# Performance work log

Hardware: AMD Instinct MI355X
Metric: run time of the kernel (lower is better)

Reference implementation:

```python
import jax, jax.numpy as jnp
import numpy as np

E = 128       # embedding_size
H = 4         # num_heads
D = E // H    # head_dim = 32
PAD = 16      # window_size; full window width = 2*PAD+1 = 33
B = 4
N = 8192


def setup_inputs() -> dict:
    key = jax.random.key(0)
    ks = jax.random.split(key, 9)
    s = 1.0 / np.sqrt(E)
    return {
        "q": jax.random.normal(ks[0], (B, N, E), dtype=jnp.float32),
        "Wq_w": jax.random.normal(ks[1], (E, E), dtype=jnp.float32) * s,
        "Wq_b": jax.random.normal(ks[2], (E,), dtype=jnp.float32) * s,
        "Wk_w": jax.random.normal(ks[3], (E, E), dtype=jnp.float32) * s,
        "Wk_b": jax.random.normal(ks[4], (E,), dtype=jnp.float32) * s,
        "Wv_w": jax.random.normal(ks[5], (E, E), dtype=jnp.float32) * s,
        "Wv_b": jax.random.normal(ks[6], (E,), dtype=jnp.float32) * s,
        "Wo_w": jax.random.normal(ks[7], (E, E), dtype=jnp.float32) * s,
        "Wo_b": jax.random.normal(ks[8], (E,), dtype=jnp.float32) * s,
    }


def reference(q, Wq_w, Wq_b, Wk_w, Wk_b, Wv_w, Wv_b, Wo_w, Wo_b):
    # Self-attention: k = v = q (forward defaults).
    Q = q @ Wq_w.T + Wq_b
    K = q @ Wk_w.T + Wk_b
    V = q @ Wv_w.T + Wv_b
    b, n, _ = Q.shape
    # (b, H, n, D)
    Q = Q.reshape(b, n, H, D).transpose(0, 2, 1, 3)
    K = K.reshape(b, n, H, D).transpose(0, 2, 1, 3)
    V = V.reshape(b, n, H, D).transpose(0, 2, 1, 3)
    W = 2 * PAD + 1
    # Zero-pad the sequence dim (matches F.pad: padded keys are zero vectors,
    # included in softmax WITHOUT masking — faithful to the original).
    K_pad = jnp.pad(K, ((0, 0), (0, 0), (PAD, PAD), (0, 0)))
    V_pad = jnp.pad(V, ((0, 0), (0, 0), (PAD, PAD), (0, 0)))
    # Window gather indices: row n sees padded positions n .. n+2*PAD
    idx = jnp.arange(n)[:, None] + jnp.arange(W)[None, :]  # (n, W)
    K_win = K_pad[:, :, idx]  # (b, H, n, W, D)
    V_win = V_pad[:, :, idx]  # (b, H, n, W, D)
    scores = jnp.einsum("bhnd,bhnwd->bhnw", Q, K_win) / jnp.sqrt(
        jnp.asarray(D, dtype=Q.dtype)
    )
    probs = jax.nn.softmax(scores, axis=-1)  # dropout is identity in eval
    out = jnp.einsum("bhnw,bhnwd->bhnd", probs, V_win)
    out = out.transpose(0, 2, 1, 3).reshape(b, n, E)
    out = out @ Wo_w.T + Wo_b
    return out, probs
```

## Files before the change

kernel.cpp:

```cpp
#include <hip/hip_runtime.h>

#define BN 4
#define NN 8192
#define EE 128
#define HH 4
#define DD 32
#define WW 33
#define MROWS (BN*NN)
#define QELEMS (MROWS*EE)
#define WELEMS (EE*EE)

typedef __bf16 bf16x8 __attribute__((ext_vector_type(8)));
typedef float f32x4 __attribute__((ext_vector_type(4)));
typedef unsigned short u16x8 __attribute__((ext_vector_type(8)));

static __device__ __forceinline__ unsigned short f2bf(float x){
    unsigned u = __float_as_uint(x);
    u += 0x7fffu + ((u >> 16) & 1u);
    return (unsigned short)(u >> 16);
}
static __device__ __forceinline__ float bf2f(unsigned short h){
    return __uint_as_float(((unsigned)h) << 16);
}
static __device__ __forceinline__ bf16x8 ld_bf8(const unsigned short* p){
    u16x8 v = *(const u16x8*)p;
    return __builtin_bit_cast(bf16x8, v);
}

__global__ void __launch_bounds__(256) prep_w(const float* __restrict__ wq, const float* __restrict__ wk,
        const float* __restrict__ wv, const float* __restrict__ wo,
        unsigned short* __restrict__ wh, unsigned short* __restrict__ wl){
    int i = blockIdx.x*256 + threadIdx.x;
    int sel = i >> 14;
    const float* src = (sel==0)? wq : (sel==1)? wk : (sel==2)? wv : wo;
    float x = src[i & (WELEMS-1)];
    unsigned short h = f2bf(x);
    wh[i] = h;
    wl[i] = f2bf(x - bf2f(h));
}

__global__ void __launch_bounds__(512,2) fused_kernel(
        const float* __restrict__ q,
        const unsigned short* __restrict__ wh, const unsigned short* __restrict__ wl,
        const float* __restrict__ bq, const float* __restrict__ bk, const float* __restrict__ bv_,
        const float* __restrict__ bo,
        float* __restrict__ out, float* __restrict__ probs)
{
    __shared__ float Kl[HH*96*33];
    __shared__ float Vl[HH*96*33];
    __shared__ float Ql[HH*64*33];

    const int t = threadIdx.x;
    const int wv = t >> 6;
    const int lane = t & 63;
    const int m = lane & 15, g = lane >> 4;
    const int b = blockIdx.y;
    const int n0 = blockIdx.x * 64;
    const size_t qrow0 = (size_t)b * NN;

    bf16x8 bH[3][4], bL[3][4];
    #pragma unroll
    for (int i=0;i<3;i++){
        const unsigned short* WH = wh + i*WELEMS + (size_t)(wv*16+m)*EE;
        const unsigned short* WL = wl + i*WELEMS + (size_t)(wv*16+m)*EE;
        #pragma unroll
        for (int kc=0;kc<4;kc++){
            bH[i][kc] = ld_bf8(WH + kc*32 + g*8);
            bL[i][kc] = ld_bf8(WL + kc*32 + g*8);
        }
    }
    const float bias3[3] = { bq[wv*16+m], bk[wv*16+m], bv_[wv*16+m] };
    const int head = wv >> 1, dimb = (wv & 1) * 16;

    float4 fa[2][8];
    {
        int grow = n0 - 16 + m;
        bool ok = (grow >= 0) && (grow < NN);
        const float* qp = q + (qrow0 + (ok ? grow : 0))*EE;
        #pragma unroll
        for (int kc=0;kc<4;kc++){
            fa[0][kc*2]   = ok ? *(const float4*)(qp + kc*32 + g*8)     : make_float4(0.f,0.f,0.f,0.f);
            fa[0][kc*2+1] = ok ? *(const float4*)(qp + kc*32 + g*8 + 4) : make_float4(0.f,0.f,0.f,0.f);
        }
    }
    #pragma unroll
    for (int tile=0; tile<6; tile++){
        if (tile < 5){
            int grow = n0 - 16 + (tile+1)*16 + m;
            bool ok = (grow >= 0) && (grow < NN);
            const float* qp = q + (qrow0 + (ok ? grow : 0))*EE;
            #pragma unroll
            for (int kc=0;kc<4;kc++){
                fa[(tile+1)&1][kc*2]   = ok ? *(const float4*)(qp + kc*32 + g*8)     : make_float4(0.f,0.f,0.f,0.f);
                fa[(tile+1)&1][kc*2+1] = ok ? *(const float4*)(qp + kc*32 + g*8 + 4) : make_float4(0.f,0.f,0.f,0.f);
            }
        }
        bf16x8 aH[4], aL[4];
        #pragma unroll
        for (int kc=0;kc<4;kc++){
            float4 v0 = fa[tile&1][kc*2], v1 = fa[tile&1][kc*2+1];
            float vvv[8] = {v0.x,v0.y,v0.z,v0.w,v1.x,v1.y,v1.z,v1.w};
            u16x8 hh, ll;
            #pragma unroll
            for (int j=0;j<8;j++){
                unsigned short hB = f2bf(vvv[j]);
                hh[j] = hB;
                ll[j] = f2bf(vvv[j] - bf2f(hB));
            }
            aH[kc] = __builtin_bit_cast(bf16x8, hh);
            aL[kc] = __builtin_bit_cast(bf16x8, ll);
        }
        #pragma unroll
        for (int i=0;i<3;i++){
            if (i==0 && (tile==0 || tile==5)) continue;
            f32x4 acc = {0.f,0.f,0.f,0.f};
            #pragma unroll
            for (int kc=0;kc<4;kc++){
                acc = __builtin_amdgcn_mfma_f32_16x16x32_bf16(aH[kc], bH[i][kc], acc, 0,0,0);
                acc = __builtin_amdgcn_mfma_f32_16x16x32_bf16(aH[kc], bL[i][kc], acc, 0,0,0);
                acc = __builtin_amdgcn_mfma_f32_16x16x32_bf16(aL[kc], bH[i][kc], acc, 0,0,0);
            }
            #pragma unroll
            for (int r=0;r<4;r++){
                int hrow = tile*16 + g*4 + r;
                int grow = n0 - 16 + hrow;
                bool inr = (grow >= 0) && (grow < NN);
                float val = acc[r] + (inr ? bias3[i] : 0.f);
                if (i==0)      Ql[(head*64 + hrow-16)*33 + dimb + m] = val;
                else if (i==1) Kl[(head*96 + hrow   )*33 + dimb + m] = val;
                else           Vl[(head*96 + hrow   )*33 + dimb + m] = val;
            }
        }
    }
    __syncthreads();

    const int pr = t >> 1, e = t & 1;
    const int p = pr & 63, h = pr >> 6;
    float qr[16];
    {
        const float* qlp = &Ql[(h*64 + p)*33 + e*16];
        #pragma unroll
        for (int k=0;k<16;k++) qr[k] = qlp[k];
    }
    float sc[WW];
    #pragma unroll
    for (int ww=0; ww<WW; ww++){
        const float* kr = &Kl[(h*96 + p + ww)*33 + e*16];
        float s = 0.f;
        #pragma unroll
        for (int k=0;k<16;k++) s = fmaf(qr[k], kr[k], s);
        sc[ww] = s;
    }
    #pragma unroll
    for (int ww=0; ww<WW; ww++)
        sc[ww] = (sc[ww] + __shfl_xor(sc[ww], 1)) * 0.17677669529663687f;

    __syncthreads();

    float mx = sc[0];
    #pragma unroll
    for (int ww=1;ww<WW;ww++) mx = fmaxf(mx, sc[ww]);
    float sum = 0.f;
    #pragma unroll
    for (int ww=0;ww<WW;ww++){ sc[ww] = __expf(sc[ww]-mx); sum += sc[ww]; }
    float inv = 1.f / sum;
    #pragma unroll
    for (int ww=0;ww<WW;ww++) sc[ww] *= inv;

    float* Pst = Ql;
    {
        float* pl = Pst + (h*64 + p)*33;
        if (e==0){
            #pragma unroll
            for (int ww=0;ww<17;ww++) pl[ww] = sc[ww];
        } else {
            #pragma unroll
            for (int ww=17;ww<WW;ww++) pl[ww] = sc[ww];
        }
    }

    float pv[16];
    #pragma unroll
    for (int k=0;k<16;k++) pv[k]=0.f;
    #pragma unroll
    for (int ww=0;ww<WW;ww++){
        const float* vr = &Vl[(h*96 + p + ww)*33 + e*16];
        float pw = sc[ww];
        #pragma unroll
        for (int k=0;k<16;k++) pv[k] = fmaf(pw, vr[k], pv[k]);
    }

    unsigned int* Au = (unsigned int*)Kl;
    {
        unsigned int* ap = Au + p*132 + h*32 + e*16;
        #pragma unroll
        for (int k=0;k<16;k++){
            unsigned short hB = f2bf(pv[k]);
            unsigned short lB = f2bf(pv[k] - bf2f(hB));
            ap[k] = ((unsigned)hB << 16) | (unsigned)lB;
        }
    }
    __syncthreads();

    bf16x8 cH[4], cL[4];
    {
        const unsigned short* WH = wh + 3*WELEMS + (size_t)(wv*16+m)*EE;
        const unsigned short* WL = wl + 3*WELEMS + (size_t)(wv*16+m)*EE;
        #pragma unroll
        for (int kc=0;kc<4;kc++){
            cH[kc] = ld_bf8(WH + kc*32 + g*8);
            cL[kc] = ld_bf8(WL + kc*32 + g*8);
        }
    }
    const float bov = bo[wv*16+m];

    #pragma unroll
    for (int i2=0;i2<17;i2++){
        int idx = t + i2*512;
        if (idx < HH*64*WW){
            int hh2 = idx / (64*WW);
            int rr  = idx - hh2*(64*WW);
            probs[((size_t)(b*HH + hh2)*NN + n0)*WW + rr] = Pst[idx];
        }
    }

    #pragma unroll
    for (int rt=0; rt<4; rt++){
        bf16x8 aH2[4], aL2[4];
        const unsigned int* ap = Au + (rt*16 + m)*132;
        #pragma unroll
        for (int kc=0;kc<4;kc++){
            const unsigned int* app = ap + kc*32 + g*8;
            u16x8 hh, ll;
            #pragma unroll
            for (int j=0;j<8;j++){
                unsigned int u = app[j];
                hh[j] = (unsigned short)(u >> 16);
                ll[j] = (unsigned short)(u & 0xffffu);
            }
            aH2[kc] = __builtin_bit_cast(bf16x8, hh);
            aL2[kc] = __builtin_bit_cast(bf16x8, ll);
        }
        f32x4 acc2 = {0.f,0.f,0.f,0.f};
        #pragma unroll
        for (int kc=0;kc<4;kc++){
            acc2 = __builtin_amdgcn_mfma_f32_16x16x32_bf16(aH2[kc], cH[kc], acc2, 0,0,0);
            acc2 = __builtin_amdgcn_mfma_f32_16x16x32_bf16(aH2[kc], cL[kc], acc2, 0,0,0);
            acc2 = __builtin_amdgcn_mfma_f32_16x16x32_bf16(aL2[kc], cH[kc], acc2, 0,0,0);
        }
        float* op = out + (qrow0 + n0 + rt*16 + g*4)*EE + wv*16 + m;
        #pragma unroll
        for (int r=0;r<4;r++) op[(size_t)r*EE] = acc2[r] + bov;
    }
}

extern "C" void kernel_launch(void* const* d_in, const int* in_sizes, int n_in,
                              void* d_out, int out_size, void* d_ws, size_t ws_size,
                              hipStream_t stream) {
    const float* q  = (const float*)d_in[0];
    const float* Wq = (const float*)d_in[1];  const float* bq = (const float*)d_in[2];
    const float* Wk = (const float*)d_in[3];  const float* bk = (const float*)d_in[4];
    const float* Wv = (const float*)d_in[5];  const float* bv = (const float*)d_in[6];
    const float* Wo = (const float*)d_in[7];  const float* bo = (const float*)d_in[8];

    float* out   = (float*)d_out;
    float* probs = out + QELEMS;

    unsigned short* w_hi = (unsigned short*)d_ws;
    unsigned short* w_lo = w_hi + 4*WELEMS;

    prep_w<<<4*WELEMS/256, 256, 0, stream>>>(Wq, Wk, Wv, Wo, w_hi, w_lo);
    fused_kernel<<<dim3(NN/64, BN), 512, 0, stream>>>(q, w_hi, w_lo,
                                                      bq, bk, bv, bo, out, probs);
}
```

Measured before the change: 149.7 us.

## Store Q/K/V as packed bf16 in LDS, split window across thread pair

Q, K and V projections are rounded to single bf16 and packed two per word in shared memory, which shrinks LDS use and allows four blocks per CU instead of two. Each thread pair now splits the 33-wide window rather than the head dimension, using vectorized 128-bit LDS reads and shuffle-reduced softmax statistics. Probabilities are written straight from registers to global memory, and the attention output feeds the output projection as one bf16 term instead of a hi/lo split, dropping one MFMA per step. This lowers precision of Q/K/V and the attention output, which risks accuracy against the fp32 reference.

```diff
diff --git a/kernel.cpp b/kernel.cpp
--- a/kernel.cpp
+++ b/kernel.cpp
@@ -6,13 +6,13 @@
 #define HH 4
 #define DD 32
 #define WW 33
-#define MROWS (BN*NN)
-#define QELEMS (MROWS*EE)
+#define QELEMS (BN*NN*EE)
 #define WELEMS (EE*EE)
 
 typedef __bf16 bf16x8 __attribute__((ext_vector_type(8)));
 typedef float f32x4 __attribute__((ext_vector_type(4)));
 typedef unsigned short u16x8 __attribute__((ext_vector_type(8)));
+typedef unsigned int u32x4 __attribute__((ext_vector_type(4)));
 
 static __device__ __forceinline__ unsigned short f2bf(float x){
     unsigned u = __float_as_uint(x);
@@ -22,6 +22,8 @@
 static __device__ __forceinline__ float bf2f(unsigned short h){
     return __uint_as_float(((unsigned)h) << 16);
 }
+static __device__ __forceinline__ float bflo(unsigned u){ return __uint_as_float(u << 16); }
+static __device__ __forceinline__ float bfhi(unsigned u){ return __uint_as_float(u & 0xffff0000u); }
 static __device__ __forceinline__ bf16x8 ld_bf8(const unsigned short* p){
     u16x8 v = *(const u16x8*)p;
     return __builtin_bit_cast(bf16x8, v);
@@ -39,16 +41,17 @@
     wl[i] = f2bf(x - bf2f(h));
 }
 
-__global__ void __launch_bounds__(512,2) fused_kernel(
+__global__ void __launch_bounds__(512,4) fused_kernel(
         const float* __restrict__ q,
         const unsigned short* __restrict__ wh, const unsigned short* __restrict__ wl,
         const float* __restrict__ bq, const float* __restrict__ bk, const float* __restrict__ bv_,
         const float* __restrict__ bo,
         float* __restrict__ out, float* __restrict__ probs)
 {
-    __shared__ float Kl[HH*96*33];
-    __shared__ float Vl[HH*96*33];
-    __shared__ float Ql[HH*64*33];
+    __shared__ unsigned int L[20480];
+    unsigned int* Kp = L;
+    unsigned int* Vp = L + 7680;
+    unsigned int* Qp = L + 15360;
 
     const int t = threadIdx.x;
     const int wv = t >> 6;
@@ -70,7 +73,8 @@
         }
     }
     const float bias3[3] = { bq[wv*16+m], bk[wv*16+m], bv_[wv*16+m] };
-    const int head = wv >> 1, dimb = (wv & 1) * 16;
+    const int head = wv >> 1;
+    const int ucol = (wv & 1)*8 + (m >> 1);
 
     float4 fa[2][8];
     {
@@ -126,9 +130,14 @@
                 int grow = n0 - 16 + hrow;
                 bool inr = (grow >= 0) && (grow < NN);
                 float val = acc[r] + (inr ? bias3[i] : 0.f);
-                if (i==0)      Ql[(head*64 + hrow-16)*33 + dimb + m] = val;
-                else if (i==1) Kl[(head*96 + hrow   )*33 + dimb + m] = val;
-                else           Vl[(head*96 + hrow   )*33 + dimb + m] = val;
+                unsigned own = f2bf(val);
+                unsigned nb  = (unsigned)__shfl_xor((int)own, 1);
+                if (!(lane & 1)){
+                    unsigned pk = own | (nb << 16);
+                    if (i==0)      Qp[(head*64 + hrow-16)*20 + ucol] = pk;
+                    else if (i==1) Kp[(head*96 + hrow   )*20 + ucol] = pk;
+                    else           Vp[(head*96 + hrow   )*20 + ucol] = pk;
+                }
             }
         }
     }
@@ -136,69 +145,106 @@
 
     const int pr = t >> 1, e = t & 1;
     const int p = pr & 63, h = pr >> 6;
-    float qr[16];
-    {
-        const float* qlp = &Ql[(h*64 + p)*33 + e*16];
-        #pragma unroll
-        for (int k=0;k<16;k++) qr[k] = qlp[k];
-    }
-    float sc[WW];
-    #pragma unroll
-    for (int ww=0; ww<WW; ww++){
-        const float* kr = &Kl[(h*96 + p + ww)*33 + e*16];
-        float s = 0.f;
-        #pragma unroll
-        for (int k=0;k<16;k++) s = fmaf(qr[k], kr[k], s);
-        sc[ww] = s;
-    }
-    #pragma unroll
-    for (int ww=0; ww<WW; ww++)
-        sc[ww] = (sc[ww] + __shfl_xor(sc[ww], 1)) * 0.17677669529663687f;
-
+
+    float qf[32];
+    {
+        const unsigned int* qb = Qp + (h*64 + p)*20;
+        #pragma unroll
+        for (int i=0;i<4;i++){
+            u32x4 v = *(const u32x4*)(qb + i*4);
+            #pragma unroll
+            for (int j=0;j<4;j++){
+                qf[i*8 + j*2]     = bflo(v[j]);
+                qf[i*8 + j*2 + 1] = bfhi(v[j]);
+            }
+        }
+    }
     __syncthreads();
 
-    float mx = sc[0];
-    #pragma unroll
-    for (int ww=1;ww<WW;ww++) mx = fmaxf(mx, sc[ww]);
-    float sum = 0.f;
-    #pragma unroll
-    for (int ww=0;ww<WW;ww++){ sc[ww] = __expf(sc[ww]-mx); sum += sc[ww]; }
-    float inv = 1.f / sum;
-    #pragma unroll
-    for (int ww=0;ww<WW;ww++) sc[ww] *= inv;
-
-    float* Pst = Ql;
-    {
-        float* pl = Pst + (h*64 + p)*33;
+    const int wbase = e * 17;
+    float sc[17];
+    {
+        const unsigned int* kb = Kp + (h*96 + p + wbase)*20;
+        #pragma unroll
+        for (int j=0;j<17;j++){
+            if (j==16 && e==1){ sc[16] = 0.f; continue; }
+            float s0=0.f, s1=0.f, s2=0.f, s3=0.f;
+            #pragma unroll
+            for (int i=0;i<4;i++){
+                u32x4 kv = *(const u32x4*)(kb + j*20 + i*4);
+                s0 = fmaf(qf[i*8+0], bflo(kv[0]), s0);
+                s1 = fmaf(qf[i*8+1], bfhi(kv[0]), s1);
+                s2 = fmaf(qf[i*8+2], bflo(kv[1]), s2);
+                s3 = fmaf(qf[i*8+3], bfhi(kv[1]), s3);
+                s0 = fmaf(qf[i*8+4], bflo(kv[2]), s0);
+                s1 = fmaf(qf[i*8+5], bfhi(kv[2]), s1);
+                s2 = fmaf(qf[i*8+6], bflo(kv[3]), s2);
+                s3 = fmaf(qf[i*8+7], bfhi(kv[3]), s3);
+            }
+            sc[j] = ((s0+s1)+(s2+s3)) * 0.17677669529663687f;
+        }
+    }
+    float mloc = -1e30f;
+    #pragma unroll
+    for (int j=0;j<17;j++){ if (j==16 && e==1) continue; mloc = fmaxf(mloc, sc[j]); }
+    float mall = fmaxf(mloc, __shfl_xor(mloc, 1));
+    float sloc = 0.f;
+    #pragma unroll
+    for (int j=0;j<17;j++){ if (j==16 && e==1) continue; sc[j] = __expf(sc[j]-mall); sloc += sc[j]; }
+    float inv = 1.f / (sloc + __shfl_xor(sloc, 1));
+    #pragma unroll
+    for (int j=0;j<17;j++) sc[j] *= inv;
+
+    {
+        float* pp = probs + ((size_t)(b*HH + h)*NN + n0 + p)*WW + wbase;
+        #pragma unroll
+        for (int j=0;j<16;j++) pp[j] = sc[j];
+        if (e==0) pp[16] = sc[16];
+    }
+
+    float pv[32];
+    #pragma unroll
+    for (int k=0;k<32;k++) pv[k] = 0.f;
+    {
+        const unsigned int* vb = Vp + (h*96 + p + wbase)*20;
+        #pragma unroll
+        for (int j=0;j<17;j++){
+            if (j==16 && e==1) continue;
+            float pw = sc[j];
+            #pragma unroll
+            for (int i=0;i<4;i++){
+                u32x4 vx = *(const u32x4*)(vb + j*20 + i*4);
+                pv[i*8+0] = fmaf(pw, bflo(vx[0]), pv[i*8+0]);
+                pv[i*8+1] = fmaf(pw, bfhi(vx[0]), pv[i*8+1]);
+                pv[i*8+2] = fmaf(pw, bflo(vx[1]), pv[i*8+2]);
+                pv[i*8+3] = fmaf(pw, bfhi(vx[1]), pv[i*8+3]);
+                pv[i*8+4] = fmaf(pw, bflo(vx[2]), pv[i*8+4]);
+                pv[i*8+5] = fmaf(pw, bfhi(vx[2]), pv[i*8+5]);
+                pv[i*8+6] = fmaf(pw, bflo(vx[3]), pv[i*8+6]);
+                pv[i*8+7] = fmaf(pw, bfhi(vx[3]), pv[i*8+7]);
+            }
+        }
+    }
+    #pragma unroll
+    for (int k=0;k<32;k++) pv[k] += __shfl_xor(pv[k], 1);
+
+    unsigned int* Ao = Qp;
+    {
+        u32x4 a0, a1;
         if (e==0){
             #pragma unroll
-            for (int ww=0;ww<17;ww++) pl[ww] = sc[ww];
+            for (int k=0;k<4;k++) a0[k] = (unsigned)f2bf(pv[2*k])   | ((unsigned)f2bf(pv[2*k+1])   << 16);
+            #pragma unroll
+            for (int k=0;k<4;k++) a1[k] = (unsigned)f2bf(pv[8+2*k]) | ((unsigned)f2bf(pv[8+2*k+1]) << 16);
         } else {
             #pragma unroll
-            for (int ww=17;ww<WW;ww++) pl[ww] = sc[ww];
-        }
-    }
-
-    float pv[16];
-    #pragma unroll
-    for (int k=0;k<16;k++) pv[k]=0.f;
-    #pragma unroll
-    for (int ww=0;ww<WW;ww++){
-        const float* vr = &Vl[(h*96 + p + ww)*33 + e*16];
-        float pw = sc[ww];
-        #pragma unroll
-        for (int k=0;k<16;k++) pv[k] = fmaf(pw, vr[k], pv[k]);
-    }
-
-    unsigned int* Au = (unsigned int*)Kl;
-    {
-        unsigned int* ap = Au + p*132 + h*32 + e*16;
-        #pragma unroll
-        for (int k=0;k<16;k++){
-            unsigned short hB = f2bf(pv[k]);
-            unsigned short lB = f2bf(pv[k] - bf2f(hB));
-            ap[k] = ((unsigned)hB << 16) | (unsigned)lB;
-        }
+            for (int k=0;k<4;k++) a0[k] = (unsigned)f2bf(pv[16+2*k]) | ((unsigned)f2bf(pv[16+2*k+1]) << 16);
+            #pragma unroll
+            for (int k=0;k<4;k++) a1[k] = (unsigned)f2bf(pv[24+2*k]) | ((unsigned)f2bf(pv[24+2*k+1]) << 16);
+        }
+        unsigned int* ap = Ao + p*68 + h*16 + e*8;
+        *(u32x4*)(ap)     = a0;
+        *(u32x4*)(ap + 4) = a1;
     }
     __syncthreads();
 
@@ -215,38 +261,14 @@
     const float bov = bo[wv*16+m];
 
     #pragma unroll
-    for (int i2=0;i2<17;i2++){
-        int idx = t + i2*512;
-        if (idx < HH*64*WW){
-            int hh2 = idx / (64*WW);
-            int rr  = idx - hh2*(64*WW);
-            probs[((size_t)(b*HH + hh2)*NN + n0)*WW + rr] = Pst[idx];
-        }
-    }
-
-    #pragma unroll
     for (int rt=0; rt<4; rt++){
-        bf16x8 aH2[4], aL2[4];
-        const unsigned int* ap = Au + (rt*16 + m)*132;
-        #pragma unroll
-        for (int kc=0;kc<4;kc++){
-            const unsigned int* app = ap + kc*32 + g*8;
-            u16x8 hh, ll;
-            #pragma unroll
-            for (int j=0;j<8;j++){
-                unsigned int u = app[j];
-                hh[j] = (unsigned short)(u >> 16);
-                ll[j] = (unsigned short)(u & 0xffffu);
-            }
-            aH2[kc] = __builtin_bit_cast(bf16x8, hh);
-            aL2[kc] = __builtin_bit_cast(bf16x8, ll);
-        }
         f32x4 acc2 = {0.f,0.f,0.f,0.f};
         #pragma unroll
         for (int kc=0;kc<4;kc++){
-            acc2 = __builtin_amdgcn_mfma_f32_16x16x32_bf16(aH2[kc], cH[kc], acc2, 0,0,0);
-            acc2 = __builtin_amdgcn_mfma_f32_16x16x32_bf16(aH2[kc], cL[kc], acc2, 0,0,0);
-            acc2 = __builtin_amdgcn_mfma_f32_16x16x32_bf16(aL2[kc], cH[kc], acc2, 0,0,0);
+            u32x4 a4 = *(const u32x4*)(Ao + (rt*16+m)*68 + kc*16 + g*4);
+            bf16x8 afr = __builtin_bit_cast(bf16x8, a4);
+            acc2 = __builtin_amdgcn_mfma_f32_16x16x32_bf16(afr, cH[kc], acc2, 0,0,0);
+            acc2 = __builtin_amdgcn_mfma_f32_16x16x32_bf16(afr, cL[kc], acc2, 0,0,0);
         }
         float* op = out + (qrow0 + n0 + rt*16 + g*4)*EE + wv*16 + m;
         #pragma unroll
```

Measured after the change: 395.1 us. +164.0%, slower.
